# Kernel tuning notes

Hardware: AMD Instinct MI355X
Metric: run time of the kernel (lower is better)

## Reference

```python
import jax, jax.numpy as jnp
import numpy as np

N_NODES = 500000
N_GRAPHS = 10000
NIN = 128
NOUT = 128
EPS = 1e-5


def setup_inputs() -> dict:
    key = jax.random.key(0)
    ks = jax.random.split(key, 10)
    x = jax.random.normal(ks[0], (N_NODES, NIN), dtype=jnp.float32)
    edge_index = jax.random.randint(ks[1], (2, 1000), 0, N_NODES, dtype=jnp.int64)
    edge_attr = jax.random.normal(ks[2], (1000, NIN), dtype=jnp.float32)
    batch = jnp.sort(jax.random.randint(ks[3], (N_NODES,), 0, N_GRAPHS, dtype=jnp.int64))
    s = 1.0 / np.sqrt(NIN)
    W_lin = jax.random.uniform(ks[4], (NIN, NIN), jnp.float32, -s, s)  # Linear(nin, nin, bias=False)
    bn_g = jnp.ones((NIN,), jnp.float32)
    bn_b = jnp.zeros((NIN,), jnp.float32)
    # MLP(nin, nout, nlayer=2, with_final_activation=False): Lin->BN->ReLU->Lin
    W1 = jax.random.uniform(ks[5], (NIN, NOUT), jnp.float32, -s, s)
    b1 = jax.random.uniform(ks[6], (NOUT,), jnp.float32, -s, s)
    bn1_g = jnp.ones((NOUT,), jnp.float32)
    bn1_b = jnp.zeros((NOUT,), jnp.float32)
    so = 1.0 / np.sqrt(NOUT)
    W2 = jax.random.uniform(ks[7], (NOUT, NOUT), jnp.float32, -so, so)
    b2 = jax.random.uniform(ks[8], (NOUT,), jnp.float32, -so, so)
    return {"x": x, "edge_index": edge_index, "edge_attr": edge_attr, "batch": batch,
            "W_lin": W_lin, "bn_g": bn_g, "bn_b": bn_b,
            "W1": W1, "b1": b1, "bn1_g": bn1_g, "bn1_b": bn1_b, "W2": W2, "b2": b2}


def _batchnorm(v, g, b):
    # training-mode BatchNorm1d: biased variance over dim 0
    mu = jnp.mean(v, axis=0, keepdims=True)
    var = jnp.mean(jnp.square(v - mu), axis=0, keepdims=True)
    return (v - mu) * jax.lax.rsqrt(var + EPS) * g + b


def reference(x, edge_index, edge_attr, batch, W_lin, bn_g, bn_b, W1, b1, bn1_g, bn1_b, W2, b2):
    # scatter-sum pooling: [num_graphs, nin]
    summation = jax.ops.segment_sum(x, batch, num_segments=N_GRAPHS)
    summation = summation @ W_lin.T if False else summation @ W_lin  # stored as [in,out]
    summation = jax.nn.relu(_batchnorm(summation, bn_g, bn_b))
    h = x + summation[batch]  # gather-broadcast add back to nodes
    # 2-layer MLP, no final activation
    h = jax.nn.relu(_batchnorm(h @ W1 + b1, bn1_g, bn1_b))
    return h @ W2 + b2
```

## Files before the change

kernel.cpp:

```cpp
#include <hip/hip_runtime.h>
#include <hip/hip_bf16.h>
#include <cstdint>
#include <cstddef>

#define NN 500000
#define NG 10000
#define F  128
#define EPSV 1e-5f

typedef __attribute__((ext_vector_type(8))) short short8;
typedef __attribute__((ext_vector_type(4))) float floatx4;

__device__ __forceinline__ short bfs(float f) {
    __hip_bfloat16 h = __float2bfloat16(f);
    union { __hip_bfloat16 h; unsigned short u; } c; c.h = h;
    return (short)c.u;
}
__device__ __forceinline__ int getb(const int* __restrict__ b, int i, int is64) {
    return is64 ? b[2 * i] : b[i];
}

__global__ void k_detect(const int* __restrict__ batch, int* __restrict__ flag) {
    __shared__ int nz;
    if (threadIdx.x == 0) nz = 0;
    __syncthreads();
    int j = 100001 + threadIdx.x * 1500;
    if (batch[j] != 0) atomicAdd(&nz, 1);
    __syncthreads();
    if (threadIdx.x == 0) flag[0] = (nz == 0) ? 1 : 0;
}

__global__ void k_bounds(const int* __restrict__ batch, int* __restrict__ gs, int* __restrict__ ge,
                         const int* __restrict__ flag) {
    int is64 = flag[0];
    int i = blockIdx.x * 256 + threadIdx.x;
    if (i >= NN) return;
    int b = getb(batch, i, is64);
    if (i == 0      || getb(batch, i - 1, is64) != b) gs[b] = i;
    if (i == NN - 1 || getb(batch, i + 1, is64) != b) ge[b] = i + 1;
}

__global__ void k_segsum(const float* __restrict__ x, const int* __restrict__ gs,
                         const int* __restrict__ ge, float* __restrict__ S) {
    __shared__ float red[8][128];
    int g = blockIdx.x;
    int s = gs[g], e = ge[g];
    int o = threadIdx.x & 31, rl = threadIdx.x >> 5;
    float acc[4] = {0.f, 0.f, 0.f, 0.f};
    for (int r = s + rl; r < e; r += 8) {
        float4 v = *reinterpret_cast<const float4*>(x + (size_t)r * F + o * 4);
        acc[0] += v.x; acc[1] += v.y; acc[2] += v.z; acc[3] += v.w;
    }
#pragma unroll
    for (int j = 0; j < 4; j++) red[rl][o * 4 + j] = acc[j];
    __syncthreads();
    if (threadIdx.x < 128) {
        float ssum = 0.f;
#pragma unroll
        for (int rr = 0; rr < 8; rr++) ssum += red[rr][threadIdx.x];
        S[(size_t)g * F + threadIdx.x] = ssum;
    }
}

__global__ void k_rowmm(const float* __restrict__ A, const float* __restrict__ W,
                        const float* __restrict__ bias, float* __restrict__ out, int hasBias) {
    int r = blockIdx.x * 2 + (threadIdx.x >> 7);
    int c = threadIdx.x & 127;
    const float* a = A + (size_t)r * F;
    float acc = hasBias ? bias[c] : 0.f;
#pragma unroll 4
    for (int k = 0; k < F; k++) acc += a[k] * W[k * F + c];
    out[(size_t)r * F + c] = acc;
}

__global__ void k_colstats(const float* __restrict__ T, float* __restrict__ sum, float* __restrict__ sumsq) {
    int f = threadIdx.x;
    int lo = blockIdx.x * 157;
    int hi = lo + 157; if (hi > NG) hi = NG;
    float s = 0.f, q = 0.f;
    for (int r = lo; r < hi; r++) { float v = T[(size_t)r * F + f]; s += v; q += v * v; }
    atomicAdd(&sum[f], s); atomicAdd(&sumsq[f], q);
}

__global__ void k_bn0(const float* __restrict__ sum, const float* __restrict__ sumsq,
                      const float* __restrict__ g, const float* __restrict__ b,
                      float* __restrict__ scale, float* __restrict__ shift) {
    int f = threadIdx.x;
    float mu  = sum[f] / (float)NG;
    float var = sumsq[f] / (float)NG - mu * mu;
    float rs  = rsqrtf(var + EPSV);
    float sc  = g[f] * rs;
    scale[f] = sc; shift[f] = b[f] - mu * sc;
}

__global__ void k_bnrelu(const float* __restrict__ T, const float* __restrict__ scale,
                         const float* __restrict__ shift, float* __restrict__ S2) {
    int e = (blockIdx.x * 256 + threadIdx.x) * 4;
    float4 t = *reinterpret_cast<const float4*>(T + e);
    int c = e & 127;
    float4 o;
    o.x = fmaxf(t.x * scale[c]     + shift[c],     0.f);
    o.y = fmaxf(t.y * scale[c + 1] + shift[c + 1], 0.f);
    o.z = fmaxf(t.z * scale[c + 2] + shift[c + 2], 0.f);
    o.w = fmaxf(t.w * scale[c + 3] + shift[c + 3], 0.f);
    *reinterpret_cast<float4*>(S2 + e) = o;
}

__device__ __forceinline__ short8 ld8bf(const float* __restrict__ p) {
    float4 f0 = *reinterpret_cast<const float4*>(p);
    float4 f1 = *reinterpret_cast<const float4*>(p + 4);
    short8 r;
    r[0] = bfs(f0.x); r[1] = bfs(f0.y); r[2] = bfs(f0.z); r[3] = bfs(f0.w);
    r[4] = bfs(f1.x); r[5] = bfs(f1.y); r[6] = bfs(f1.z); r[7] = bfs(f1.w);
    return r;
}

__global__ __launch_bounds__(256, 2)
void k_pass1(const float* __restrict__ x, const int* __restrict__ batch,
             const float* __restrict__ W1, const float* __restrict__ Z,
             float* __restrict__ partials, const int* __restrict__ flag) {
    const int is64 = flag[0];
    const int lane = threadIdx.x & 63;
    const int wave = threadIdx.x >> 6;
    const int wm = wave & 1, wn = wave >> 1;
    const int quad = lane >> 4, l16 = lane & 15;

    short8 Bf[4][4];
#pragma unroll
    for (int nt = 0; nt < 4; nt++) {
        int n = wn * 64 + nt * 16 + l16;
#pragma unroll
        for (int kt = 0; kt < 4; kt++)
#pragma unroll
            for (int j = 0; j < 8; j++)
                Bf[nt][kt][j] = bfs(W1[(kt * 32 + quad * 8 + j) * F + n]);
    }

    float su[4], sq[4];
#pragma unroll
    for (int nt = 0; nt < 4; nt++) { su[nt] = 0.f; sq[nt] = 0.f; }

    const int NT = (NN + 63) / 64;
    for (int tile = blockIdx.x; tile < NT; tile += gridDim.x) {
        int rb = tile * 64 + wm * 32;
        floatx4 acc[2][4];
#pragma unroll
        for (int mt = 0; mt < 2; mt++)
#pragma unroll
            for (int nt = 0; nt < 4; nt++) acc[mt][nt] = (floatx4){0.f, 0.f, 0.f, 0.f};

#pragma unroll
        for (int kt = 0; kt < 4; kt++) {
            short8 A[2];
#pragma unroll
            for (int mt = 0; mt < 2; mt++) {
                int r = rb + mt * 16 + l16; if (r >= NN) r = NN - 1;
                A[mt] = ld8bf(x + (size_t)r * F + kt * 32 + quad * 8);
            }
#pragma unroll
            for (int mt = 0; mt < 2; mt++)
#pragma unroll
                for (int nt = 0; nt < 4; nt++)
                    acc[mt][nt] = __builtin_amdgcn_mfma_f32_16x16x32_bf16(A[mt], Bf[nt][kt], acc[mt][nt], 0, 0, 0);
        }

#pragma unroll
        for (int mt = 0; mt < 2; mt++)
#pragma unroll
            for (int reg = 0; reg < 4; reg++) {
                int r = rb + mt * 16 + quad * 4 + reg;
                bool valid = r < NN;
                int g = getb(batch, valid ? r : NN - 1, is64);
                const float* zr = Z + (size_t)g * F + wn * 64 + l16;
#pragma unroll
                for (int nt = 0; nt < 4; nt++) {
                    float u = acc[mt][nt][reg] + zr[nt * 16];
                    if (valid) { su[nt] += u; sq[nt] += u * u; }
                }
            }
    }

    float* ps = partials + (size_t)(blockIdx.x & 63) * 256;
#pragma unroll
    for (int nt = 0; nt < 4; nt++) {
        float s = su[nt], q = sq[nt];
        s += __shfl_xor(s, 16, 64); s += __shfl_xor(s, 32, 64);
        q += __shfl_xor(q, 16, 64); q += __shfl_xor(q, 32, 64);
        if (quad == 0) {
            int col = wn * 64 + nt * 16 + l16;
            atomicAdd(&ps[col], s);
            atomicAdd(&ps[128 + col], q);
        }
    }
}

__global__ void k_bn1(const float* __restrict__ partials, const float* __restrict__ g1,
                      const float* __restrict__ b1g, float* __restrict__ scale1,
                      float* __restrict__ shift1) {
    int f = threadIdx.x;
    float s = 0.f, q = 0.f;
    for (int t = 0; t < 64; t++) { s += partials[t * 256 + f]; q += partials[t * 256 + 128 + f]; }
    float mu  = s / (float)NN;
    float var = q / (float)NN - mu * mu;
    float rs  = rsqrtf(var + EPSV);
    float sc  = g1[f] * rs;
    scale1[f] = sc; shift1[f] = b1g[f] - mu * sc;
}

__global__ __launch_bounds__(256, 2)
void k_pass2(const float* __restrict__ x, const int* __restrict__ batch,
             const float* __restrict__ W1, const float* __restrict__ W2,
             const float* __restrict__ Z, const float* __restrict__ scale1,
             const float* __restrict__ shift1, const float* __restrict__ b2,
             float* __restrict__ out, const int* __restrict__ flag) {
    extern __shared__ unsigned short h2[];
    const int is64 = flag[0];
    const int lane = threadIdx.x & 63;
    const int wave = threadIdx.x >> 6;
    const int wm = wave & 1, wn = wave >> 1;
    const int quad = lane >> 4, l16 = lane & 15;

    short8 Bf1[4][4], Bf2[4][4];
    float sc1[4], sh1[4], bb2[4];
#pragma unroll
    for (int nt = 0; nt < 4; nt++) {
        int n = wn * 64 + nt * 16 + l16;
        sc1[nt] = scale1[n]; sh1[nt] = shift1[n]; bb2[nt] = b2[n];
#pragma unroll
        for (int kt = 0; kt < 4; kt++)
#pragma unroll
            for (int j = 0; j < 8; j++) {
                int k = kt * 32 + quad * 8 + j;
                Bf1[nt][kt][j] = bfs(W1[k * F + n]);
                Bf2[nt][kt][j] = bfs(W2[k * F + n]);
            }
    }

    const int NT = (NN + 63) / 64;
    for (int tile = blockIdx.x; tile < NT; tile += gridDim.x) {
        int rb = tile * 64 + wm * 32;
        floatx4 acc[2][4];
#pragma unroll
        for (int mt = 0; mt < 2; mt++)
#pragma unroll
            for (int nt = 0; nt < 4; nt++) acc[mt][nt] = (floatx4){0.f, 0.f, 0.f, 0.f};

#pragma unroll
        for (int kt = 0; kt < 4; kt++) {
            short8 A[2];
#pragma unroll
            for (int mt = 0; mt < 2; mt++) {
                int r = rb + mt * 16 + l16; if (r >= NN) r = NN - 1;
                A[mt] = ld8bf(x + (size_t)r * F + kt * 32 + quad * 8);
            }
#pragma unroll
            for (int mt = 0; mt < 2; mt++)
#pragma unroll
                for (int nt = 0; nt < 4; nt++)
                    acc[mt][nt] = __builtin_amdgcn_mfma_f32_16x16x32_bf16(A[mt], Bf1[nt][kt], acc[mt][nt], 0, 0, 0);
        }

        __syncthreads();
#pragma unroll
        for (int mt = 0; mt < 2; mt++)
#pragma unroll
            for (int reg = 0; reg < 4; reg++) {
                int lr = wm * 32 + mt * 16 + quad * 4 + reg;
                int r = tile * 64 + lr; if (r >= NN) r = NN - 1;
                int g = getb(batch, r, is64);
                const float* zr = Z + (size_t)g * F + wn * 64 + l16;
#pragma unroll
                for (int nt = 0; nt < 4; nt++) {
                    float u = acc[mt][nt][reg] + zr[nt * 16];
                    float h = fmaxf(u * sc1[nt] + sh1[nt], 0.f);
                    h2[lr * 136 + wn * 64 + nt * 16 + l16] = (unsigned short)bfs(h);
                }
            }
        __syncthreads();

        floatx4 acc2[2][4];
#pragma unroll
        for (int mt = 0; mt < 2; mt++)
#pragma unroll
            for (int nt = 0; nt < 4; nt++) acc2[mt][nt] = (floatx4){0.f, 0.f, 0.f, 0.f};
#pragma unroll
        for (int kt = 0; kt < 4; kt++) {
            short8 A2[2];
#pragma unroll
            for (int mt = 0; mt < 2; mt++)
                A2[mt] = *reinterpret_cast<const short8*>(&h2[(wm * 32 + mt * 16 + l16) * 136 + kt * 32 + quad * 8]);
#pragma unroll
            for (int mt = 0; mt < 2; mt++)
#pragma unroll
                for (int nt = 0; nt < 4; nt++)
                    acc2[mt][nt] = __builtin_amdgcn_mfma_f32_16x16x32_bf16(A2[mt], Bf2[nt][kt], acc2[mt][nt], 0, 0, 0);
        }

#pragma unroll
        for (int mt = 0; mt < 2; mt++)
#pragma unroll
            for (int reg = 0; reg < 4; reg++) {
                int r = rb + mt * 16 + quad * 4 + reg;
                if (r < NN) {
#pragma unroll
                    for (int nt = 0; nt < 4; nt++)
                        out[(size_t)r * F + wn * 64 + nt * 16 + l16] = acc2[mt][nt][reg] + bb2[nt];
                }
            }
    }
}

extern "C" void kernel_launch(void* const* d_in, const int* in_sizes, int n_in,
                              void* d_out, int out_size, void* d_ws, size_t ws_size,
                              hipStream_t stream) {
    const float* x    = (const float*)d_in[0];
    const int*   batch= (const int*)d_in[3];
    const float* Wl   = (const float*)d_in[4];
    const float* bng  = (const float*)d_in[5];
    const float* bnb  = (const float*)d_in[6];
    const float* W1   = (const float*)d_in[7];
    const float* b1   = (const float*)d_in[8];
    const float* bn1g = (const float*)d_in[9];
    const float* bn1b = (const float*)d_in[10];
    const float* W2   = (const float*)d_in[11];
    const float* b2   = (const float*)d_in[12];
    float* out = (float*)d_out;

    char* ws = (char*)d_ws;
    float* S        = (float*)(ws + 0);
    float* T        = (float*)(ws + 5120000);
    int*   gs       = (int*)  (ws + 10240000);
    int*   ge       = (int*)  (ws + 10280000);
    float* sum0     = (float*)(ws + 10320000);
    float* sumsq0   = (float*)(ws + 10320512);
    float* scale0   = (float*)(ws + 10321024);
    float* shift0   = (float*)(ws + 10321536);
    float* partials = (float*)(ws + 10322048);
    float* scale1   = (float*)(ws + 10387584);
    float* shift1   = (float*)(ws + 10388096);
    int*   flag     = (int*)  (ws + 10388608);

    hipMemsetAsync(ws + 10240000, 0, 147584, stream);

    k_detect <<<1, 256, 0, stream>>>(batch, flag);
    k_bounds <<<(NN + 255) / 256, 256, 0, stream>>>(batch, gs, ge, flag);
    k_segsum <<<NG, 256, 0, stream>>>(x, gs, ge, S);
    k_rowmm  <<<NG / 2, 256, 0, stream>>>(S, Wl, nullptr, T, 0);
    k_colstats<<<64, 128, 0, stream>>>(T, sum0, sumsq0);
    k_bn0    <<<1, 128, 0, stream>>>(sum0, sumsq0, bng, bnb, scale0, shift0);
    k_bnrelu <<<NG * F / 1024, 256, 0, stream>>>(T, scale0, shift0, S);
    k_rowmm  <<<NG / 2, 256, 0, stream>>>(S, W1, b1, T, 1);
    k_pass1  <<<2048, 256, 0, stream>>>(x, batch, W1, T, partials, flag);
    k_bn1    <<<1, 128, 0, stream>>>(partials, bn1g, bn1b, scale1, shift1);
    k_pass2  <<<2048, 256, 64 * 136 * 2, stream>>>(x, batch, W1, W2, T, scale1, shift1, b2, out, flag);
}
```

Baseline: 841.6 us.

## Cache bf16 copy of x in segsum and read prepacked bf16 weights from global

The segment-sum kernel now also writes a bf16 copy of x to workspace. Both MLP passes read that half-size copy instead of re-reading and converting fp32 x. Weights are pre-transposed to bf16 fragment layout once, so B fragments are loaded from global/L2 instead of held in registers, and launch bounds rise to 4 blocks per SM for more occupancy. Pass2 double-buffers its LDS staging tile. This needs a much larger workspace (falls back to the old path otherwise) and adds one extra write of x.

```diff
diff --git a/kernel.cpp b/kernel.cpp
--- a/kernel.cpp
+++ b/kernel.cpp
@@ -41,7 +41,8 @@
 }
 
 __global__ void k_segsum(const float* __restrict__ x, const int* __restrict__ gs,
-                         const int* __restrict__ ge, float* __restrict__ S) {
+                         const int* __restrict__ ge, float* __restrict__ S,
+                         unsigned short* __restrict__ xb) {
     __shared__ float red[8][128];
     int g = blockIdx.x;
     int s = gs[g], e = ge[g];
@@ -50,6 +51,12 @@
     for (int r = s + rl; r < e; r += 8) {
         float4 v = *reinterpret_cast<const float4*>(x + (size_t)r * F + o * 4);
         acc[0] += v.x; acc[1] += v.y; acc[2] += v.z; acc[3] += v.w;
+        if (xb) {
+            ushort4 bv;
+            bv.x = (unsigned short)bfs(v.x); bv.y = (unsigned short)bfs(v.y);
+            bv.z = (unsigned short)bfs(v.z); bv.w = (unsigned short)bfs(v.w);
+            *reinterpret_cast<ushort4*>(xb + (size_t)r * F + o * 4) = bv;
+        }
     }
 #pragma unroll
     for (int j = 0; j < 4; j++) red[rl][o * 4 + j] = acc[j];
@@ -60,6 +67,16 @@
         for (int rr = 0; rr < 8; rr++) ssum += red[rr][threadIdx.x];
         S[(size_t)g * F + threadIdx.x] = ssum;
     }
+}
+
+__global__ void k_wfrag(const float* __restrict__ W1, const float* __restrict__ W2,
+                        unsigned short* __restrict__ W1f, unsigned short* __restrict__ W2f) {
+    int i = blockIdx.x * 256 + threadIdx.x;
+    int sel = i >> 14, j = i & 16383;
+    int n = j >> 7, kk = j & 127;
+    const float* W = sel ? W2 : W1;
+    unsigned short* Wf = sel ? W2f : W1f;
+    Wf[j] = (unsigned short)bfs(W[kk * F + n]);
 }
 
 __global__ void k_rowmm(const float* __restrict__ A, const float* __restrict__ W,
@@ -115,9 +132,10 @@
     return r;
 }
 
-__global__ __launch_bounds__(256, 2)
-void k_pass1(const float* __restrict__ x, const int* __restrict__ batch,
-             const float* __restrict__ W1, const float* __restrict__ Z,
+
+__global__ __launch_bounds__(256, 4)
+void k_pass1(const unsigned short* __restrict__ xb, const int* __restrict__ batch,
+             const unsigned short* __restrict__ W1f, const float* __restrict__ Z,
              float* __restrict__ partials, const int* __restrict__ flag) {
     const int is64 = flag[0];
     const int lane = threadIdx.x & 63;
@@ -125,16 +143,7 @@
     const int wm = wave & 1, wn = wave >> 1;
     const int quad = lane >> 4, l16 = lane & 15;
 
-    short8 Bf[4][4];
-#pragma unroll
-    for (int nt = 0; nt < 4; nt++) {
-        int n = wn * 64 + nt * 16 + l16;
-#pragma unroll
-        for (int kt = 0; kt < 4; kt++)
-#pragma unroll
-            for (int j = 0; j < 8; j++)
-                Bf[nt][kt][j] = bfs(W1[(kt * 32 + quad * 8 + j) * F + n]);
-    }
+    const unsigned short* wbase = W1f + ((wn * 64 + l16) * F + quad * 8);
 
     float su[4], sq[4];
 #pragma unroll
@@ -155,13 +164,15 @@
 #pragma unroll
             for (int mt = 0; mt < 2; mt++) {
                 int r = rb + mt * 16 + l16; if (r >= NN) r = NN - 1;
-                A[mt] = ld8bf(x + (size_t)r * F + kt * 32 + quad * 8);
-            }
-#pragma unroll
-            for (int mt = 0; mt < 2; mt++)
-#pragma unroll
-                for (int nt = 0; nt < 4; nt++)
-                    acc[mt][nt] = __builtin_amdgcn_mfma_f32_16x16x32_bf16(A[mt], Bf[nt][kt], acc[mt][nt], 0, 0, 0);
+                A[mt] = *reinterpret_cast<const short8*>(xb + (size_t)r * F + kt * 32 + quad * 8);
+            }
+#pragma unroll
+            for (int nt = 0; nt < 4; nt++) {
+                short8 B = *reinterpret_cast<const short8*>(wbase + nt * 16 * F + kt * 32);
+#pragma unroll
+                for (int mt = 0; mt < 2; mt++)
+                    acc[mt][nt] = __builtin_amdgcn_mfma_f32_16x16x32_bf16(A[mt], B, acc[mt][nt], 0, 0, 0);
+            }
         }
 
 #pragma unroll
@@ -207,12 +218,193 @@
     scale1[f] = sc; shift1[f] = b1g[f] - mu * sc;
 }
 
-__global__ __launch_bounds__(256, 2)
-void k_pass2(const float* __restrict__ x, const int* __restrict__ batch,
-             const float* __restrict__ W1, const float* __restrict__ W2,
+__global__ __launch_bounds__(256, 4)
+void k_pass2(const unsigned short* __restrict__ xb, const int* __restrict__ batch,
+             const unsigned short* W1f, const unsigned short* W2f,
              const float* __restrict__ Z, const float* __restrict__ scale1,
              const float* __restrict__ shift1, const float* __restrict__ b2,
-             float* __restrict__ out, const int* __restrict__ flag) {
+             float* out, const int* __restrict__ flag) {
+    __shared__ unsigned short h2[2][64][136];
+    const int is64 = flag[0];
+    const int lane = threadIdx.x & 63;
+    const int wave = threadIdx.x >> 6;
+    const int wm = wave & 1, wn = wave >> 1;
+    const int quad = lane >> 4, l16 = lane & 15;
+
+    float sc1[4], sh1[4], bb2[4];
+#pragma unroll
+    for (int nt = 0; nt < 4; nt++) {
+        int n = wn * 64 + nt * 16 + l16;
+        sc1[nt] = scale1[n]; sh1[nt] = shift1[n]; bb2[nt] = b2[n];
+    }
+    const unsigned short* w1base = W1f + ((wn * 64 + l16) * F + quad * 8);
+    const unsigned short* w2base = W2f + ((wn * 64 + l16) * F + quad * 8);
+
+    int buf = 0;
+    const int NT = (NN + 63) / 64;
+    for (int tile = blockIdx.x; tile < NT; tile += gridDim.x) {
+        int rb = tile * 64 + wm * 32;
+        floatx4 acc[2][4];
+#pragma unroll
+        for (int mt = 0; mt < 2; mt++)
+#pragma unroll
+            for (int nt = 0; nt < 4; nt++) acc[mt][nt] = (floatx4){0.f, 0.f, 0.f, 0.f};
+
+#pragma unroll
+        for (int kt = 0; kt < 4; kt++) {
+            short8 A[2];
+#pragma unroll
+            for (int mt = 0; mt < 2; mt++) {
+                int r = rb + mt * 16 + l16; if (r >= NN) r = NN - 1;
+                A[mt] = *reinterpret_cast<const short8*>(xb + (size_t)r * F + kt * 32 + quad * 8);
+            }
+#pragma unroll
+            for (int nt = 0; nt < 4; nt++) {
+                short8 B = *reinterpret_cast<const short8*>(w1base + nt * 16 * F + kt * 32);
+#pragma unroll
+                for (int mt = 0; mt < 2; mt++)
+                    acc[mt][nt] = __builtin_amdgcn_mfma_f32_16x16x32_bf16(A[mt], B, acc[mt][nt], 0, 0, 0);
+            }
+        }
+
+#pragma unroll
+        for (int mt = 0; mt < 2; mt++)
+#pragma unroll
+            for (int reg = 0; reg < 4; reg++) {
+                int lr = wm * 32 + mt * 16 + quad * 4 + reg;
+                int r = tile * 64 + lr; if (r >= NN) r = NN - 1;
+                int g = getb(batch, r, is64);
+                const float* zr = Z + (size_t)g * F + wn * 64 + l16;
+#pragma unroll
+                for (int nt = 0; nt < 4; nt++) {
+                    float u = acc[mt][nt][reg] + zr[nt * 16];
+                    float h = fmaxf(u * sc1[nt] + sh1[nt], 0.f);
+                    h2[buf][lr][wn * 64 + nt * 16 + l16] = (unsigned short)bfs(h);
+                }
+            }
+        __syncthreads();
+
+        floatx4 acc2[2][4];
+#pragma unroll
+        for (int mt = 0; mt < 2; mt++)
+#pragma unroll
+            for (int nt = 0; nt < 4; nt++) acc2[mt][nt] = (floatx4){0.f, 0.f, 0.f, 0.f};
+#pragma unroll
+        for (int kt = 0; kt < 4; kt++) {
+            short8 A2[2];
+#pragma unroll
+            for (int mt = 0; mt < 2; mt++)
+                A2[mt] = *reinterpret_cast<const short8*>(&h2[buf][wm * 32 + mt * 16 + l16][kt * 32 + quad * 8]);
+#pragma unroll
+            for (int nt = 0; nt < 4; nt++) {
+                short8 B = *reinterpret_cast<const short8*>(w2base + nt * 16 * F + kt * 32);
+#pragma unroll
+                for (int mt = 0; mt < 2; mt++)
+                    acc2[mt][nt] = __builtin_amdgcn_mfma_f32_16x16x32_bf16(A2[mt], B, acc2[mt][nt], 0, 0, 0);
+            }
+        }
+
+#pragma unroll
+        for (int mt = 0; mt < 2; mt++)
+#pragma unroll
+            for (int reg = 0; reg < 4; reg++) {
+                int r = rb + mt * 16 + quad * 4 + reg;
+                if (r < NN) {
+#pragma unroll
+                    for (int nt = 0; nt < 4; nt++)
+                        out[(size_t)r * F + wn * 64 + nt * 16 + l16] = acc2[mt][nt][reg] + bb2[nt];
+                }
+            }
+        buf ^= 1;
+    }
+}
+
+
+__global__ __launch_bounds__(256, 2)
+void k_pass1_old(const float* __restrict__ x, const int* __restrict__ batch,
+                 const float* __restrict__ W1, const float* __restrict__ Z,
+                 float* __restrict__ partials, const int* __restrict__ flag) {
+    const int is64 = flag[0];
+    const int lane = threadIdx.x & 63;
+    const int wave = threadIdx.x >> 6;
+    const int wm = wave & 1, wn = wave >> 1;
+    const int quad = lane >> 4, l16 = lane & 15;
+
+    short8 Bf[4][4];
+#pragma unroll
+    for (int nt = 0; nt < 4; nt++) {
+        int n = wn * 64 + nt * 16 + l16;
+#pragma unroll
+        for (int kt = 0; kt < 4; kt++)
+#pragma unroll
+            for (int j = 0; j < 8; j++)
+                Bf[nt][kt][j] = bfs(W1[(kt * 32 + quad * 8 + j) * F + n]);
+    }
+
+    float su[4], sq[4];
+#pragma unroll
+    for (int nt = 0; nt < 4; nt++) { su[nt] = 0.f; sq[nt] = 0.f; }
+
+    const int NT = (NN + 63) / 64;
+    for (int tile = blockIdx.x; tile < NT; tile += gridDim.x) {
+        int rb = tile * 64 + wm * 32;
+        floatx4 acc[2][4];
+#pragma unroll
+        for (int mt = 0; mt < 2; mt++)
+#pragma unroll
+            for (int nt = 0; nt < 4; nt++) acc[mt][nt] = (floatx4){0.f, 0.f, 0.f, 0.f};
+
+#pragma unroll
+        for (int kt = 0; kt < 4; kt++) {
+            short8 A[2];
+#pragma unroll
+            for (int mt = 0; mt < 2; mt++) {
+                int r = rb + mt * 16 + l16; if (r >= NN) r = NN - 1;
+                A[mt] = ld8bf(x + (size_t)r * F + kt * 32 + quad * 8);
+            }
+#pragma unroll
+            for (int mt = 0; mt < 2; mt++)
+#pragma unroll
+                for (int nt = 0; nt < 4; nt++)
+                    acc[mt][nt] = __builtin_amdgcn_mfma_f32_16x16x32_bf16(A[mt], Bf[nt][kt], acc[mt][nt], 0, 0, 0);
+        }
+
+#pragma unroll
+        for (int mt = 0; mt < 2; mt++)
+#pragma unroll
+            for (int reg = 0; reg < 4; reg++) {
+                int r = rb + mt * 16 + quad * 4 + reg;
+                bool valid = r < NN;
+                int g = getb(batch, valid ? r : NN - 1, is64);
+                const float* zr = Z + (size_t)g * F + wn * 64 + l16;
+#pragma unroll
+                for (int nt = 0; nt < 4; nt++) {
+                    float u = acc[mt][nt][reg] + zr[nt * 16];
+                    if (valid) { su[nt] += u; sq[nt] += u * u; }
+                }
+            }
+    }
+
+    float* ps = partials + (size_t)(blockIdx.x & 63) * 256;
+#pragma unroll
+    for (int nt = 0; nt < 4; nt++) {
+        float s = su[nt], q = sq[nt];
+        s += __shfl_xor(s, 16, 64); s += __shfl_xor(s, 32, 64);
+        q += __shfl_xor(q, 16, 64); q += __shfl_xor(q, 32, 64);
+        if (quad == 0) {
+            int col = wn * 64 + nt * 16 + l16;
+            atomicAdd(&ps[col], s);
+            atomicAdd(&ps[128 + col], q);
+        }
+    }
+}
+
+__global__ __launch_bounds__(256, 2)
+void k_pass2_old(const float* __restrict__ x, const int* __restrict__ batch,
+                 const float* __restrict__ W1, const float* __restrict__ W2,
+                 const float* __restrict__ Z, const float* __restrict__ scale1,
+                 const float* __restrict__ shift1, const float* __restrict__ b2,
+                 float* __restrict__ out, const int* __restrict__ flag) {
     extern __shared__ unsigned short h2[];
     const int is64 = flag[0];
     const int lane = threadIdx.x & 63;
@@ -325,32 +517,82 @@
     const float* W2   = (const float*)d_in[11];
     const float* b2   = (const float*)d_in[12];
     float* out = (float*)d_out;
-
     char* ws = (char*)d_ws;
-    float* S        = (float*)(ws + 0);
-    float* T        = (float*)(ws + 5120000);
-    int*   gs       = (int*)  (ws + 10240000);
-    int*   ge       = (int*)  (ws + 10280000);
-    float* sum0     = (float*)(ws + 10320000);
-    float* sumsq0   = (float*)(ws + 10320512);
-    float* scale0   = (float*)(ws + 10321024);
-    float* shift0   = (float*)(ws + 10321536);
-    float* partials = (float*)(ws + 10322048);
-    float* scale1   = (float*)(ws + 10387584);
-    float* shift1   = (float*)(ws + 10388096);
-    int*   flag     = (int*)  (ws + 10388608);
-
-    hipMemsetAsync(ws + 10240000, 0, 147584, stream);
-
-    k_detect <<<1, 256, 0, stream>>>(batch, flag);
-    k_bounds <<<(NN + 255) / 256, 256, 0, stream>>>(batch, gs, ge, flag);
-    k_segsum <<<NG, 256, 0, stream>>>(x, gs, ge, S);
-    k_rowmm  <<<NG / 2, 256, 0, stream>>>(S, Wl, nullptr, T, 0);
-    k_colstats<<<64, 128, 0, stream>>>(T, sum0, sumsq0);
-    k_bn0    <<<1, 128, 0, stream>>>(sum0, sumsq0, bng, bnb, scale0, shift0);
-    k_bnrelu <<<NG * F / 1024, 256, 0, stream>>>(T, scale0, shift0, S);
-    k_rowmm  <<<NG / 2, 256, 0, stream>>>(S, W1, b1, T, 1);
-    k_pass1  <<<2048, 256, 0, stream>>>(x, batch, W1, T, partials, flag);
-    k_bn1    <<<1, 128, 0, stream>>>(partials, bn1g, bn1b, scale1, shift1);
-    k_pass2  <<<2048, 256, 64 * 136 * 2, stream>>>(x, batch, W1, W2, T, scale1, shift1, b2, out, flag);
-}
+
+    const size_t OFF_XB     = 0;
+    const size_t OFF_W1F    = 128000000;
+    const size_t OFF_W2F    = 128032768;
+    const size_t OFF_S      = 128065536;
+    const size_t OFF_T      = 133185536;
+    const size_t OFF_GS     = 138305536;
+    const size_t OFF_GE     = 138345536;
+    const size_t OFF_SUM0   = 138385536;
+    const size_t OFF_SUMSQ0 = 138386048;
+    const size_t OFF_SCALE0 = 138386560;
+    const size_t OFF_SHIFT0 = 138387072;
+    const size_t OFF_PART   = 138387584;
+    const size_t OFF_SCALE1 = 138453120;
+    const size_t OFF_SHIFT1 = 138453632;
+    const size_t OFF_FLAG   = 138454144;
+    const size_t NEED       = 138454148;
+
+    if (ws_size >= NEED) {
+        unsigned short* xb  = (unsigned short*)(ws + OFF_XB);
+        unsigned short* W1f = (unsigned short*)(ws + OFF_W1F);
+        unsigned short* W2f = (unsigned short*)(ws + OFF_W2F);
+        float* S        = (float*)(ws + OFF_S);
+        float* T        = (float*)(ws + OFF_T);
+        int*   gs       = (int*)  (ws + OFF_GS);
+        int*   ge       = (int*)  (ws + OFF_GE);
+        float* sum0     = (float*)(ws + OFF_SUM0);
+        float* sumsq0   = (float*)(ws + OFF_SUMSQ0);
+        float* scale0   = (float*)(ws + OFF_SCALE0);
+        float* shift0   = (float*)(ws + OFF_SHIFT0);
+        float* partials = (float*)(ws + OFF_PART);
+        float* scale1   = (float*)(ws + OFF_SCALE1);
+        float* shift1   = (float*)(ws + OFF_SHIFT1);
+        int*   flag     = (int*)  (ws + OFF_FLAG);
+
+        hipMemsetAsync(ws + OFF_GS, 0, NEED - OFF_GS, stream);
+
+        k_detect <<<1, 256, 0, stream>>>(batch, flag);
+        k_wfrag  <<<128, 256, 0, stream>>>(W1, W2, W1f, W2f);
+        k_bounds <<<(NN + 255) / 256, 256, 0, stream>>>(batch, gs, ge, flag);
+        k_segsum <<<NG, 256, 0, stream>>>(x, gs, ge, S, xb);
+        k_rowmm  <<<NG / 2, 256, 0, stream>>>(S, Wl, nullptr, T, 0);
+        k_colstats<<<64, 128, 0, stream>>>(T, sum0, sumsq0);
+        k_bn0    <<<1, 128, 0, stream>>>(sum0, sumsq0, bng, bnb, scale0, shift0);
+        k_bnrelu <<<NG * F / 1024, 256, 0, stream>>>(T, scale0, shift0, S);
+        k_rowmm  <<<NG / 2, 256, 0, stream>>>(S, W1, b1, T, 1);
+        k_pass1  <<<2048, 256, 0, stream>>>(xb, batch, W1f, T, partials, flag);
+        k_bn1    <<<1, 128, 0, stream>>>(partials, bn1g, bn1b, scale1, shift1);
+        k_pass2  <<<2048, 256, 0, stream>>>(xb, batch, W1f, W2f, T, scale1, shift1, b2, out, flag);
+    } else {
+        float* S        = (float*)(ws + 0);
+        float* T        = (float*)(ws + 5120000);
+        int*   gs       = (int*)  (ws + 10240000);
+        int*   ge       = (int*)  (ws + 10280000);
+        float* sum0     = (float*)(ws + 10320000);
+        float* sumsq0   = (float*)(ws + 10320512);
+        float* scale0   = (float*)(ws + 10321024);
+        float* shift0   = (float*)(ws + 10321536);
+        float* partials = (float*)(ws + 10322048);
+        float* scale1   = (float*)(ws + 10387584);
+        float* shift1   = (float*)(ws + 10388096);
+        int*   flag     = (int*)  (ws + 10388608);
+
+        hipMemsetAsync(ws + 10240000, 0, 147584, stream);
+
+        k_detect <<<1, 256, 0, stream>>>(batch, flag);
+        k_bounds <<<(NN + 255) / 256, 256, 0, stream>>>(batch, gs, ge, flag);
+        k_segsum <<<NG, 256, 0, stream>>>(x, gs, ge, S, nullptr);
+        k_rowmm  <<<NG / 2, 256, 0, stream>>>(S, Wl, nullptr, T, 0);
+        k_colstats<<<64, 128, 0, stream>>>(T, sum0, sumsq0);
+        k_bn0    <<<1, 128, 0, stream>>>(sum0, sumsq0, bng, bnb, scale0, shift0);
+        k_bnrelu <<<NG * F / 1024, 256, 0, stream>>>(T, scale0, shift0, S);
+        k_rowmm  <<<NG / 2, 256, 0, stream>>>(S, W1, b1, T, 1);
+        k_pass1_old <<<2048, 256, 0, stream>>>(x, batch, W1, T, partials, flag);
+        k_bn1    <<<1, 128, 0, stream>>>(partials, bn1g, bn1b, scale1, shift1);
+        k_pass2_old <<<2048, 256, 64 * 136 * 2, stream>>>(x, batch, W1, W2, T, scale1, shift1, b2, out, flag);
+    }
+}
```

New measurement: 889.2 us. 5.7% more time.
